# Performance work log

Measured on AMD Instinct MI355X. Metric: run time of the kernel, lower is better.

Reference implementation:

```python
import jax, jax.numpy as jnp
import numpy as np

ALPHA_MARGIN = 1.0


def setup_inputs() -> dict:
    key = jax.random.key(0)
    k1, k2 = jax.random.split(key)
    B, N, H = 32, 128, 128  # batch, num_node, num_hidden
    X = jax.random.normal(k1, (B, N * N, 2 * H), dtype=jnp.float32)
    y = jax.random.randint(k2, (B, N, N), 0, 2, dtype=jnp.int32)
    return {"X": X, "y": y}


def reference(X, y):
    B, P, D = X.shape
    H = D // 2
    # split pair embeddings: e_a = X[..., :H], e_b = X[..., H:]
    diff = X[:, :, :H] - X[:, :, H:]
    dist2 = jnp.sum(diff * diff, axis=-1)  # (B, N*N) squared L2 distance
    adj = y.reshape(B, P)  # pair i corresponds to (i // N, i % N) == row-major flatten
    pos_loss = dist2
    neg_loss = jnp.maximum(ALPHA_MARGIN - dist2, 0.0)
    # entries untouched by the original loop (adj not in {0,1}) remain 0
    loss = jnp.where(adj == 1, pos_loss, jnp.where(adj == 0, neg_loss, 0.0))
    return loss
```

## Files before the change

### kernel.cpp

```cpp
#include <hip/hip_runtime.h>
#include <hip/hip_bf16.h>

#define ALPHA_MARGIN 1.0f

__global__ __launch_bounds__(256) void closs_kernel(
        const float4* __restrict__ X4,
        const int*    __restrict__ y,
        float*        __restrict__ out,
        int n_pairs) {
    int wave = (int)((blockIdx.x * blockDim.x + threadIdx.x) >> 6);
    int lane = threadIdx.x & 63;
    if (wave >= n_pairs) return;

    float4 v = X4[(size_t)wave * 64 + lane];

    float ox = __shfl_xor(v.x, 32);
    float oy = __shfl_xor(v.y, 32);
    float oz = __shfl_xor(v.z, 32);
    float ow = __shfl_xor(v.w, 32);

    float dx = v.x - ox;
    float dy = v.y - oy;
    float dz = v.z - oz;
    float dw = v.w - ow;
    float s = dx * dx + dy * dy + dz * dz + dw * dw;

    #pragma unroll
    for (int m = 16; m >= 1; m >>= 1)
        s += __shfl_xor(s, m);

    if (lane == 0) {
        int adj = y[wave];
        float loss;
        if (adj == 1)      loss = s;
        else if (adj == 0) loss = fmaxf(ALPHA_MARGIN - s, 0.0f);
        else               loss = 0.0f;
        out[wave] = loss;
    }
}

extern "C" void kernel_launch(void* const* d_in, const int* in_sizes, int n_in,
                              void* d_out, int out_size, void* d_ws, size_t ws_size,
                              hipStream_t stream) {
    const float* X = (const float*)d_in[0];
    const int*   y = (const int*)d_in[1];
    float* out = (float*)d_out;

    int n_pairs = in_sizes[1];
    int blocks = (n_pairs + 3) / 4;

    closs_kernel<<<blocks, 256, 0, stream>>>((const float4*)X, y, out, n_pairs);
}
```

Baseline: 666.9 us.

## Process two pairs per wavefront with grid-stride loop and capped grid

Each wavefront now handles two pairs at once, with each half-wave loading the a and b halves of its own pair directly instead of exchanging across halves by shuffle. The kernel becomes a grid-stride loop over a grid capped at 2048 blocks, which cuts block launch overhead and the cross-half shuffles. The cost is fewer blocks resident in flight to hide memory latency. Each half-wave load now covers 512 contiguous bytes rather than 1 KB, so coalescing changes slightly.

```diff
diff --git a/kernel.cpp b/kernel.cpp
--- a/kernel.cpp
+++ b/kernel.cpp
@@ -1,5 +1,4 @@
 #include <hip/hip_runtime.h>
-#include <hip/hip_bf16.h>
 
 #define ALPHA_MARGIN 1.0f
 
@@ -8,34 +7,37 @@
         const int*    __restrict__ y,
         float*        __restrict__ out,
         int n_pairs) {
-    int wave = (int)((blockIdx.x * blockDim.x + threadIdx.x) >> 6);
-    int lane = threadIdx.x & 63;
-    if (wave >= n_pairs) return;
+    const int lane = threadIdx.x & 63;
+    const int h    = lane >> 5;
+    const int i    = lane & 31;
+    const int wave = (int)((blockIdx.x * blockDim.x + threadIdx.x) >> 6);
+    const int nwav = (int)((gridDim.x * blockDim.x) >> 6);
 
-    float4 v = X4[(size_t)wave * 64 + lane];
+    for (int p0 = wave * 2; p0 < n_pairs; p0 += nwav * 2) {
+        const int p = p0 + h;
+        if (p < n_pairs) {
+            const size_t base = (size_t)p * 64;
+            float4 va = X4[base + i];
+            float4 vb = X4[base + 32 + i];
+            float dx = va.x - vb.x;
+            float dy = va.y - vb.y;
+            float dz = va.z - vb.z;
+            float dw = va.w - vb.w;
+            float s = dx * dx + dy * dy + dz * dz + dw * dw;
 
-    float ox = __shfl_xor(v.x, 32);
-    float oy = __shfl_xor(v.y, 32);
-    float oz = __shfl_xor(v.z, 32);
-    float ow = __shfl_xor(v.w, 32);
+            #pragma unroll
+            for (int m = 16; m >= 1; m >>= 1)
+                s += __shfl_xor(s, m);
 
-    float dx = v.x - ox;
-    float dy = v.y - oy;
-    float dz = v.z - oz;
-    float dw = v.w - ow;
-    float s = dx * dx + dy * dy + dz * dz + dw * dw;
-
-    #pragma unroll
-    for (int m = 16; m >= 1; m >>= 1)
-        s += __shfl_xor(s, m);
-
-    if (lane == 0) {
-        int adj = y[wave];
-        float loss;
-        if (adj == 1)      loss = s;
-        else if (adj == 0) loss = fmaxf(ALPHA_MARGIN - s, 0.0f);
-        else               loss = 0.0f;
-        out[wave] = loss;
+            if (i == 0) {
+                int adj = y[p];
+                float loss;
+                if (adj == 1)      loss = s;
+                else if (adj == 0) loss = fmaxf(ALPHA_MARGIN - s, 0.0f);
+                else               loss = 0.0f;
+                out[p] = loss;
+            }
+        }
     }
 }
 
@@ -47,7 +49,9 @@
     float* out = (float*)d_out;
 
     int n_pairs = in_sizes[1];
-    int blocks = (n_pairs + 3) / 4;
+
+    int blocks = (n_pairs + 7) / 8;
+    if (blocks > 2048) blocks = 2048;
 
     closs_kernel<<<blocks, 256, 0, stream>>>((const float4*)X, y, out, n_pairs);
 }
```

New measurement: 671.4 us. Within noise of the previous version (+0.7%).
